# Kernel optimization log

Hardware: AMD Instinct MI355X
Metric: run time of the kernel (lower is better)

Reference implementation:

```python
import jax, jax.numpy as jnp
import numpy as np

B, H_IMG, W_IMG = 2, 192, 192
DIM, HEADS, WS, SHIFT = 192, 6, 8, 4
MLP_HID = 4 * DIM
EPS = 1e-5


def _rel_pos_index(ws):
    coords = np.stack(np.meshgrid(np.arange(ws), np.arange(ws), indexing='ij'))  # (2, ws, ws)
    cf = coords.reshape(2, -1)
    rel = (cf[:, :, None] - cf[:, None, :]).transpose(1, 2, 0)  # (ww, ww, 2)
    rel[:, :, 0] += ws - 1
    rel[:, :, 1] += ws - 1
    rel[:, :, 0] *= 2 * ws - 1
    return jnp.asarray(rel.sum(-1))  # (ww, ww) int


def _attn_mask(h, w, ws, shift):
    img = np.zeros((h, w))
    cnt = 0
    for hs in (slice(0, -ws), slice(-ws, -shift), slice(-shift, None)):
        for wsl in (slice(0, -ws), slice(-ws, -shift), slice(-shift, None)):
            img[hs, wsl] = cnt
            cnt += 1
    mw = img.reshape(h // ws, ws, w // ws, ws).transpose(0, 2, 1, 3).reshape(-1, ws * ws)
    am = mw[:, None, :] - mw[:, :, None]
    return jnp.asarray(np.where(am != 0, -100.0, 0.0), dtype=jnp.float32)


def setup_inputs() -> dict:
    key = jax.random.key(0)
    ks = jax.random.split(key, 16)
    n = H_IMG * W_IMG
    std = 0.02
    inp = {
        'x_left': jax.random.normal(ks[0], (B, n, DIM), jnp.float32),
        'x_right': jax.random.normal(ks[1], (B, n, DIM), jnp.float32),
        'd_left': jax.random.uniform(ks[2], (B, H_IMG, W_IMG), jnp.float32) * 8.0,
        'd_right': jax.random.uniform(ks[3], (B, H_IMG, W_IMG), jnp.float32) * 8.0,
        'norm1_g': jnp.ones((DIM,), jnp.float32),
        'norm1_b': jnp.zeros((DIM,), jnp.float32),
        'q_w': jax.random.normal(ks[4], (DIM, DIM), jnp.float32) * std,
        'q_b': jnp.zeros((DIM,), jnp.float32),
        'kv_w': jax.random.normal(ks[5], (DIM, 2 * DIM), jnp.float32) * std,
        'kv_b': jnp.zeros((2 * DIM,), jnp.float32),
        'proj_w': jax.random.normal(ks[6], (DIM, DIM), jnp.float32) * std,
        'proj_b': jnp.zeros((DIM,), jnp.float32),
        'rel_bias_table': jax.random.normal(ks[7], ((2 * WS - 1) ** 2, HEADS), jnp.float32) * std,
        'norm2_g': jnp.ones((DIM,), jnp.float32),
        'norm2_b': jnp.zeros((DIM,), jnp.float32),
        'fc1_w': jax.random.normal(ks[8], (DIM, MLP_HID), jnp.float32) * std,
        'fc1_b': jnp.zeros((MLP_HID,), jnp.float32),
        'fc2_w': jax.random.normal(ks[9], (MLP_HID, DIM), jnp.float32) * std,
        'fc2_b': jnp.zeros((DIM,), jnp.float32),
        'h': H_IMG,
        'w': W_IMG,
    }
    return inp


def _forward(x_left, x_right, d_left, d_right,
             norm1_g, norm1_b, q_w, q_b, kv_w, kv_b, proj_w, proj_b,
             rel_bias_table, norm2_g, norm2_b, fc1_w, fc1_b, fc2_w, fc2_b,
             h, w):
    b, n, c = x_left.shape
    ws, shift, heads = WS, SHIFT, HEADS
    hd = c // heads
    scale = hd ** -0.5
    ww = ws * ws
    nW = (h // ws) * (w // ws)

    rel_idx = _rel_pos_index(ws)
    # (heads, ww, ww) gathered relative-position bias
    bias = rel_bias_table[rel_idx.reshape(-1)].reshape(ww, ww, heads).transpose(2, 0, 1)
    mask = _attn_mask(h, w, ws, shift)  # (nW, ww, ww)

    coords_w = jnp.arange(w, dtype=jnp.float32)[None, None, :]
    r2l = jnp.clip(coords_w + 0.5 - d_left, 0.0, None).astype(jnp.int32)
    l2r = jnp.clip(coords_w + 0.5 + d_right, None, float(w - 1)).astype(jnp.int32)

    def ln(x, g, bt):
        mu = x.mean(-1, keepdims=True)
        var = ((x - mu) ** 2).mean(-1, keepdims=True)
        return (x - mu) / jnp.sqrt(var + EPS) * g + bt

    sc_l, sc_r = x_left, x_right
    xl = ln(x_left, norm1_g, norm1_b).reshape(b, h, w, c)
    xr = ln(x_right, norm1_g, norm1_b).reshape(b, h, w, c)
    # epipolar gather along width
    xl_sel = jnp.take_along_axis(xl, l2r[..., None], axis=2)
    xr_sel = jnp.take_along_axis(xr, r2l[..., None], axis=2)

    def shift_f(x):
        return jnp.roll(x, (-shift, -shift), axis=(1, 2))

    def part(x):  # window partition -> (b*nW, ww, c)
        x = x.reshape(b, h // ws, ws, w // ws, ws, c).transpose(0, 1, 3, 2, 4, 5)
        return x.reshape(-1, ww, c)

    xlw, xrw = part(shift_f(xl)), part(shift_f(xr))
    xlsw, xrsw = part(shift_f(xl_sel)), part(shift_f(xr_sel))

    def win_attn(xq, xkv):
        B_ = xq.shape[0]
        q = (xq @ q_w + q_b).reshape(B_, ww, heads, hd).transpose(0, 2, 1, 3) * scale
        kv = (xkv @ kv_w + kv_b).reshape(B_, ww, 2, heads, hd).transpose(2, 0, 3, 1, 4)
        k, v = kv[0], kv[1]
        a = jnp.einsum('bhqd,bhkd->bhqk', q, k) + bias[None]
        a = a.reshape(B_ // nW, nW, heads, ww, ww) + mask[None, :, None]
        a = jax.nn.softmax(a.reshape(B_, heads, ww, ww), axis=-1)
        o = jnp.einsum('bhqk,bhkd->bqhd', a, v).reshape(B_, ww, c)
        return o @ proj_w + proj_b, a

    xlT, a_r2l = win_attn(xlw, xrsw)
    xrT, a_l2r = win_attn(xrw, xlsw)

    def m_relax(M, p=2):  # sum over +-p shifts along the query axis
        out = M
        for i in range(1, p + 1):
            out = out + jnp.pad(M[:, :, :-i, :], ((0, 0), (0, 0), (i, 0), (0, 0)))
            out = out + jnp.pad(M[:, :, i:, :], ((0, 0), (0, 0), (0, i), (0, 0)))
        return out

    m_l = jnp.einsum('bhik,bhki->bhi', m_relax(a_r2l), a_l2r)
    m_r = jnp.einsum('bhik,bhki->bhi', m_relax(a_l2r), a_r2l)
    m_l = jax.lax.stop_gradient(jnp.tanh(5.0 * m_l.transpose(0, 2, 1)[..., None]))  # (B_, ww, heads, 1)
    m_r = jax.lax.stop_gradient(jnp.tanh(5.0 * m_r.transpose(0, 2, 1)[..., None]))

    def fuse(x_orig, x_t, m):
        B_ = x_orig.shape[0]
        xo = x_orig.reshape(B_, ww, heads, hd)
        xt = x_t.reshape(B_, ww, heads, hd)
        return (xo * (1.0 - m) + xt * m).reshape(B_, ww, c)

    xlT = fuse(xlw, xlT, m_l)
    xrT = fuse(xrw, xrT, m_r)

    def rev(win):  # window reverse + roll back
        x = win.reshape(b, h // ws, w // ws, ws, ws, c).transpose(0, 1, 3, 2, 4, 5).reshape(b, h, w, c)
        return jnp.roll(x, (shift, shift), axis=(1, 2))

    xl_out = sc_l + rev(xlT).reshape(b, n, c)
    xr_out = sc_r + rev(xrT).reshape(b, n, c)

    def mlp(x):
        return jax.nn.gelu(x @ fc1_w + fc1_b, approximate=False) @ fc2_w + fc2_b

    xl_out = xl_out + mlp(ln(xl_out, norm2_g, norm2_b))
    xr_out = xr_out + mlp(ln(xr_out, norm2_g, norm2_b))
    return xl_out, xr_out


def reference(x_left, x_right, d_left, d_right,
              norm1_g, norm1_b, q_w, q_b, kv_w, kv_b, proj_w, proj_b,
              rel_bias_table, norm2_g, norm2_b, fc1_w, fc1_b, fc2_w, fc2_b,
              h, w):
    return _forward(x_left, x_right, d_left, d_right,
                    norm1_g, norm1_b, q_w, q_b, kv_w, kv_b, proj_w, proj_b,
                    rel_bias_table, norm2_g, norm2_b, fc1_w, fc1_b, fc2_w, fc2_b,
                    h, w)
```

## Files before the change

### kernel.cpp

```cpp
#include <hip/hip_runtime.h>
#include <hip/hip_bf16.h>

#define BB 2
#define HH 192
#define WIMG 192
#define CC 192
#define NHEADS 6
#define HD 32
#define NTOK (HH*WIMG)
#define NWX 24
#define NWIN 576
#define BWIN (BB*NWIN)
#define MLPH 768
#define EPS_ 1e-5f
#define NSIDE_TOK (BB*NTOK)

typedef __attribute__((ext_vector_type(8))) short bf16x8;
typedef __attribute__((ext_vector_type(4))) float f32x4;

#define GLOBAL_AS __attribute__((address_space(1)))
#define LDS_AS __attribute__((address_space(3)))
__device__ __forceinline__ void gll16(const void* g, void* l) {
    __builtin_amdgcn_global_load_lds((const GLOBAL_AS unsigned int*)g,
                                     (LDS_AS unsigned int*)l, 16, 0, 0);
}

__device__ __forceinline__ unsigned short f2bf(float f) {
    __hip_bfloat16 h = __float2bfloat16(f);
    return *reinterpret_cast<unsigned short*>(&h);
}
__device__ __forceinline__ float bfu(unsigned short u) {
    return __uint_as_float(((unsigned int)u) << 16);
}
__device__ __forceinline__ float gelu_fast(float x) {
    float z = 1.5957691216f*(x + 0.044715f*x*x*x);
    float e = __expf(z);
    float t = 1.0f - 2.0f/(e + 1.0f);
    return 0.5f*x*(1.0f + t);
}
__device__ __forceinline__ int tokof(int b, int wi, int wj, int p) {
    int rh = wi*8 + (p>>3), rw = wj*8 + (p&7);
    int i = rh + 4; if (i >= HH) i -= HH;
    int j = rw + 4; if (j >= WIMG) j -= WIMG;
    return b*NTOK + i*WIMG + j;
}

__global__ __launch_bounds__(256) void ln1_kernel(
    const float* __restrict__ xl, const float* __restrict__ xr,
    const float* __restrict__ g, const float* __restrict__ bta,
    __hip_bfloat16* __restrict__ xln_all)
{
    int token = blockIdx.x*4 + (threadIdx.x >> 6);
    int lane = threadIdx.x & 63;
    const float* src;
    __hip_bfloat16* dst;
    if (token < NSIDE_TOK) { src = xl + (size_t)token*CC; dst = xln_all + (size_t)token*CC; }
    else { int t2 = token - NSIDE_TOK; src = xr + (size_t)t2*CC; dst = xln_all + (size_t)token*CC; }
    float v0 = src[lane], v1 = src[lane+64], v2 = src[lane+128];
    float s = v0+v1+v2;
    float q = v0*v0 + v1*v1 + v2*v2;
    #pragma unroll
    for (int m = 32; m; m >>= 1) { s += __shfl_xor(s, m, 64); q += __shfl_xor(q, m, 64); }
    float mu = s * (1.0f/CC);
    float inv = rsqrtf(fmaxf(q*(1.0f/CC) - mu*mu, 0.0f) + EPS_);
    dst[lane]     = __float2bfloat16((v0-mu)*inv*g[lane]     + bta[lane]);
    dst[lane+64]  = __float2bfloat16((v1-mu)*inv*g[lane+64]  + bta[lane+64]);
    dst[lane+128] = __float2bfloat16((v2-mu)*inv*g[lane+128] + bta[lane+128]);
}

__global__ __launch_bounds__(256) void map_kernel(
    const float* __restrict__ d_left, const float* __restrict__ d_right,
    int* __restrict__ map)
{
    int gid = blockIdx.x*256 + threadIdx.x;
    int side = (gid >= NSIDE_TOK) ? 1 : 0;
    int row = gid - side*NSIDE_TOK;
    int j = row % WIMG;
    float d = side ? d_right[row] : d_left[row];
    int jj;
    if (!side) { float f = (float)j + 0.5f - d; f = fmaxf(f, 0.f); jj = (int)f; }
    else       { float f = (float)j + 0.5f + d; f = fminf(f, 191.f); jj = (int)f; }
    map[gid] = (side ? 0 : NSIDE_TOK) + row - j + jj;
}

__global__ __launch_bounds__(256) void conv_w_kernel(
    const float* __restrict__ q_w, const float* __restrict__ kv_w,
    const float* __restrict__ proj_w, const float* __restrict__ fc1_w,
    const float* __restrict__ fc2_w,
    __hip_bfloat16* __restrict__ q_wf, __hip_bfloat16* __restrict__ kv_wf,
    __hip_bfloat16* __restrict__ proj_f, __hip_bfloat16* __restrict__ W1f,
    __hip_bfloat16* __restrict__ W2f)
{
    int idx = blockIdx.x*256 + threadIdx.x;
    if (idx < 36864) {
        int j = idx & 7, lane = (idx>>3) & 63, fr = idx>>9;
        int ct = fr % 12, ks = fr / 12;
        int n = ct*16 + (lane&15), k = ks*32 + (lane>>4)*8 + j;
        q_wf[idx] = __float2bfloat16(q_w[(size_t)k*192 + n]);
    } else if (idx < 110592) {
        int i2 = idx - 36864;
        int j = i2 & 7, lane = (i2>>3) & 63, fr = i2>>9;
        int ct = fr % 24, ks = fr / 24;
        int n = ct*16 + (lane&15), k = ks*32 + (lane>>4)*8 + j;
        kv_wf[i2] = __float2bfloat16(kv_w[(size_t)k*384 + n]);
    } else if (idx < 147456) {
        int i2 = idx - 110592;
        int j = i2 & 7, lane = (i2>>3) & 63, fr = i2>>9;
        int ct = fr % 12, h = fr / 12;
        int n = ct*16 + (lane&15), k = h*32 + (lane>>4)*8 + j;
        proj_f[i2] = __float2bfloat16(proj_w[(size_t)k*192 + n]);
    } else if (idx < 294912) {
        int i2 = idx - 147456;
        int j = i2 & 7, lane = (i2>>3) & 63, fr = i2>>9;
        int ct = fr & 1, ks = (fr>>1) % 6, cc2 = fr / 12;
        int n = cc2*32 + ct*16 + (lane&15), k = ks*32 + (lane>>4)*8 + j;
        W1f[i2] = __float2bfloat16(fc1_w[(size_t)k*MLPH + n]);
    } else {
        int i2 = idx - 294912;
        int j = i2 & 7, lane = (i2>>3) & 63, fr = i2>>9;
        int ct = fr % 12, ks = (fr/12) % 2, cc = fr / 24;
        int n = ct*16 + (lane&15), k = cc*64 + ks*32 + (lane>>4)*8 + j;
        W2f[i2] = __float2bfloat16(fc2_w[(size_t)k*192 + n]);
    }
}

__global__ __launch_bounds__(256) void bias_setup_kernel(
    const float* __restrict__ table, float* __restrict__ bias_glob)
{
    int idx = blockIdx.x*256 + threadIdx.x;
    int h = idx >> 12, rem = idx & 4095;
    int q = rem >> 6, k = rem & 63;
    int qy = q>>3, qx = q&7, ky = k>>3, kx = k&7;
    int ridx = (qy-ky+7)*15 + (qx-kx+7);
    bias_glob[idx] = table[ridx*NHEADS + h];
}

template<int NT>
__global__ __launch_bounds__(256) void proj_gemm_kernel(
    const __hip_bfloat16* __restrict__ in, const __hip_bfloat16* __restrict__ Wf,
    const float* __restrict__ bias, const int* __restrict__ map,
    __hip_bfloat16* __restrict__ outp, float scale)
{
    __shared__ unsigned short wst[2][NT*512];
    const int tid = threadIdx.x, lane = tid & 63, w = tid >> 6;
    const int r16 = lane & 15, kg = lane >> 4, w16 = w*16;
    const size_t baserow = (size_t)blockIdx.x * 64;
    const int row = (int)baserow + w16 + r16;
    const size_t arow = map ? (size_t)map[row] : (size_t)row;

    bf16x8 aReg[6];
    #pragma unroll
    for (int ks = 0; ks < 6; ++ks)
        aReg[ks] = *reinterpret_cast<const bf16x8*>(in + arow*CC + ks*32 + kg*8);

    const char* wsrc = (const char*)Wf;
    const int soff = w*1024 + lane*16;
    #pragma unroll
    for (int i = 0; i < NT/4; ++i)
        gll16(wsrc + i*4096 + soff, (char*)wst[0] + i*4096 + w*1024);

    f32x4 acc[NT];
    #pragma unroll
    for (int ct = 0; ct < NT; ++ct) { float bv = bias[ct*16+r16]; acc[ct] = (f32x4){bv,bv,bv,bv}; }

    #pragma unroll
    for (int ks = 0; ks < 6; ++ks) {
        __syncthreads();
        if (ks < 5) {
            const char* s2 = wsrc + (size_t)(ks+1)*NT*1024;
            #pragma unroll
            for (int i = 0; i < NT/4; ++i)
                gll16(s2 + i*4096 + soff, (char*)wst[(ks+1)&1] + i*4096 + w*1024);
        }
        #pragma unroll
        for (int ct = 0; ct < NT; ++ct) {
            bf16x8 bb = *reinterpret_cast<const bf16x8*>(wst[ks&1] + ct*512 + lane*8);
            acc[ct] = __builtin_amdgcn_mfma_f32_16x16x32_bf16(aReg[ks], bb, acc[ct], 0, 0, 0);
        }
    }
    const int ldo = NT*16;
    #pragma unroll
    for (int ct = 0; ct < NT; ++ct)
        #pragma unroll
        for (int r = 0; r < 4; ++r)
            outp[(baserow + w16 + kg*4 + r)*ldo + ct*16 + r16] =
                __float2bfloat16(acc[ct][r] * scale);
}

__global__ __launch_bounds__(128) void attn_pm_kernel(
    const __hip_bfloat16* __restrict__ Qglob,
    const __hip_bfloat16* __restrict__ KVglob,
    const float* __restrict__ bias_glob,
    __hip_bfloat16* __restrict__ Og,
    float* __restrict__ mg)
{
    __shared__ unsigned short Pl[2][64*72];
    __shared__ unsigned short Vl[2][32*72];
    const int tid = threadIdx.x, lane = tid & 63, s = tid >> 6;
    const int r16 = lane & 15, kg = lane >> 4;
    const int bid = blockIdx.x;
    const int wd = bid / NHEADS, h = bid % NHEADS;
    const int b = wd / NWIN, win = wd % NWIN;
    const int wi = win / NWX, wj = win % NWX;
    const bool edge_i = (wi == NWX-1), edge_j = (wj == NWX-1);

    const __hip_bfloat16* Qs  = Qglob  + (size_t)s*NSIDE_TOK*CC;
    const __hip_bfloat16* KVs = KVglob + (size_t)s*NSIDE_TOK*(2*CC);

    int tokQ[4];
    #pragma unroll
    for (int mi = 0; mi < 4; ++mi) tokQ[mi] = tokof(b, wi, wj, mi*16 + r16);
    const int tokV = tokof(b, wi, wj, lane);

    unsigned short* P = Pl[s];
    unsigned short* V = Vl[s];

    {
        bf16x8 vv[4];
        #pragma unroll
        for (int dg = 0; dg < 4; ++dg)
            vv[dg] = *reinterpret_cast<const bf16x8*>(
                KVs + (size_t)tokV*(2*CC) + CC + h*HD + dg*8);
        #pragma unroll
        for (int dg = 0; dg < 4; ++dg)
            #pragma unroll
            for (int jj = 0; jj < 8; ++jj)
                V[(dg*8+jj)*72 + lane] = (unsigned short)vv[dg][jj];
    }

    bf16x8 aQ[4], bK[4];
    #pragma unroll
    for (int mi = 0; mi < 4; ++mi)
        aQ[mi] = *reinterpret_cast<const bf16x8*>(
            Qs + (size_t)tokQ[mi]*CC + h*HD + kg*8);
    #pragma unroll
    for (int ni = 0; ni < 4; ++ni)
        bK[ni] = *reinterpret_cast<const bf16x8*>(
            KVs + (size_t)tokQ[ni]*(2*CC) + h*HD + kg*8);
    f32x4 S[4][4];
    #pragma unroll
    for (int mi = 0; mi < 4; ++mi)
        #pragma unroll
        for (int ni = 0; ni < 4; ++ni)
            S[mi][ni] = __builtin_amdgcn_mfma_f32_16x16x32_bf16(
                aQ[mi], bK[ni], (f32x4){0.f,0.f,0.f,0.f}, 0, 0, 0);

    #pragma unroll
    for (int mi = 0; mi < 4; ++mi)
        #pragma unroll
        for (int ni = 0; ni < 4; ++ni)
            #pragma unroll
            for (int rr = 0; rr < 4; ++rr) {
                int q = mi*16 + kg*4 + rr, k = ni*16 + r16;
                float bm = bias_glob[h*4096 + q*64 + k];
                int qy = q>>3, qx = q&7, ky = k>>3, kx = k&7;
                bool msk = (edge_i && ((qy<4) != (ky<4))) ||
                           (edge_j && ((qx<4) != (kx<4)));
                S[mi][ni][rr] += bm + (msk ? -100.0f : 0.0f);
            }

    float mx[4][4], sm[4][4];
    #pragma unroll
    for (int mi = 0; mi < 4; ++mi)
        #pragma unroll
        for (int rr = 0; rr < 4; ++rr)
            mx[mi][rr] = fmaxf(fmaxf(S[mi][0][rr], S[mi][1][rr]),
                               fmaxf(S[mi][2][rr], S[mi][3][rr]));
    #pragma unroll
    for (int m = 1; m <= 8; m <<= 1)
        #pragma unroll
        for (int mi = 0; mi < 4; ++mi)
            #pragma unroll
            for (int rr = 0; rr < 4; ++rr)
                mx[mi][rr] = fmaxf(mx[mi][rr], __shfl_xor(mx[mi][rr], m, 64));
    #pragma unroll
    for (int mi = 0; mi < 4; ++mi)
        #pragma unroll
        for (int rr = 0; rr < 4; ++rr) sm[mi][rr] = 0.f;
    #pragma unroll
    for (int mi = 0; mi < 4; ++mi)
        #pragma unroll
        for (int ni = 0; ni < 4; ++ni)
            #pragma unroll
            for (int rr = 0; rr < 4; ++rr) {
                S[mi][ni][rr] = __expf(S[mi][ni][rr] - mx[mi][rr]);
                sm[mi][rr] += S[mi][ni][rr];
            }
    #pragma unroll
    for (int m = 1; m <= 8; m <<= 1)
        #pragma unroll
        for (int mi = 0; mi < 4; ++mi)
            #pragma unroll
            for (int rr = 0; rr < 4; ++rr)
                sm[mi][rr] += __shfl_xor(sm[mi][rr], m, 64);
    #pragma unroll
    for (int mi = 0; mi < 4; ++mi)
        #pragma unroll
        for (int rr = 0; rr < 4; ++rr) sm[mi][rr] = 1.0f / sm[mi][rr];

    #pragma unroll
    for (int mi = 0; mi < 4; ++mi)
        #pragma unroll
        for (int ni = 0; ni < 4; ++ni)
            #pragma unroll
            for (int rr = 0; rr < 4; ++rr)
                P[(mi*16 + kg*4 + rr)*72 + ni*16 + r16] =
                    f2bf(S[mi][ni][rr] * sm[mi][rr]);

    {
        f32x4 O[4][2];
        #pragma unroll
        for (int mi = 0; mi < 4; ++mi)
            #pragma unroll
            for (int dt = 0; dt < 2; ++dt) O[mi][dt] = (f32x4){0.f,0.f,0.f,0.f};
        #pragma unroll
        for (int ks = 0; ks < 2; ++ks) {
            bf16x8 aP[4], bV[2];
            #pragma unroll
            for (int mi = 0; mi < 4; ++mi)
                aP[mi] = *reinterpret_cast<const bf16x8*>(
                    P + (mi*16 + r16)*72 + ks*32 + kg*8);
            #pragma unroll
            for (int dt = 0; dt < 2; ++dt)
                bV[dt] = *reinterpret_cast<const bf16x8*>(
                    V + (dt*16 + r16)*72 + ks*32 + kg*8);
            #pragma unroll
            for (int mi = 0; mi < 4; ++mi)
                #pragma unroll
                for (int dt = 0; dt < 2; ++dt)
                    O[mi][dt] = __builtin_amdgcn_mfma_f32_16x16x32_bf16(
                        aP[mi], bV[dt], O[mi][dt], 0, 0, 0);
        }
        __hip_bfloat16* ob = Og + ((size_t)(s*BWIN + wd)*64)*CC + h*HD;
        #pragma unroll
        for (int mi = 0; mi < 4; ++mi)
            #pragma unroll
            for (int dt = 0; dt < 2; ++dt)
                #pragma unroll
                for (int rr = 0; rr < 4; ++rr)
                    ob[(size_t)(mi*16 + kg*4 + rr)*CC + dt*16 + r16] =
                        __float2bfloat16(O[mi][dt][rr]);
    }

    __syncthreads();

    {
        const unsigned short* Pa = Pl[s];
        const unsigned short* Pb = Pl[s^1];
        const int i = lane;
        const int s0 = (i >= 2) ? -2 : -i;
        const int s1 = (i <= 61) ? 2 : 63 - i;
        float acc = 0.f;
        for (int k = 0; k < 64; k += 2) {
            float pb0 = bfu(Pb[k*72 + i]);
            float pb1 = bfu(Pb[(k+1)*72 + i]);
            float a0 = 0.f, a1 = 0.f;
            for (int ss = s0; ss <= s1; ++ss) {
                unsigned int pr = *reinterpret_cast<const unsigned int*>(
                    &Pa[(i+ss)*72 + k]);
                a0 += bfu((unsigned short)(pr & 0xffff));
                a1 += bfu((unsigned short)(pr >> 16));
            }
            acc += a0*pb0 + a1*pb1;
        }
        float e = __expf(10.0f * acc);
        mg[((size_t)(s*BWIN + wd)*NHEADS + h)*64 + i] = 1.0f - 2.0f/(e + 1.0f);
    }
}

__global__ __launch_bounds__(256) void projfuse_kernel(
    const __hip_bfloat16* __restrict__ Og,
    const __hip_bfloat16* __restrict__ proj_f,
    const float* __restrict__ proj_b,
    const float* __restrict__ mg,
    const __hip_bfloat16* __restrict__ xln_all,
    const float* __restrict__ x_left, const float* __restrict__ x_right,
    const float* __restrict__ g2, const float* __restrict__ b2,
    float* __restrict__ out, __hip_bfloat16* __restrict__ xln2)
{
    __shared__ unsigned short wst[2][12*512];
    const int tid = threadIdx.x, lane = tid & 63, w = tid >> 6;
    const int r16 = lane & 15, kg = lane >> 4, w16 = w*16;
    const int bid = blockIdx.x;
    const int s = bid / BWIN, wd = bid % BWIN;
    const int b = wd / NWIN, win = wd % NWIN;
    const int wi = win / NWX, wj = win % NWX;

    const size_t orow = (size_t)(s*BWIN + wd)*64 + w16 + r16;
    bf16x8 aReg[6];
    #pragma unroll
    for (int ks = 0; ks < 6; ++ks)
        aReg[ks] = *reinterpret_cast<const bf16x8*>(Og + orow*CC + ks*32 + kg*8);

    const char* wsrc = (const char*)proj_f;
    const int soff = w*1024 + lane*16;
    #pragma unroll
    for (int i = 0; i < 3; ++i)
        gll16(wsrc + i*4096 + soff, (char*)wst[0] + i*4096 + w*1024);

    f32x4 acc[12];
    #pragma unroll
    for (int ct = 0; ct < 12; ++ct) { float bv = proj_b[ct*16+r16]; acc[ct] = (f32x4){bv,bv,bv,bv}; }

    #pragma unroll
    for (int ks = 0; ks < 6; ++ks) {
        __syncthreads();
        if (ks < 5) {
            const char* s2 = wsrc + (size_t)(ks+1)*12288;
            #pragma unroll
            for (int i = 0; i < 3; ++i)
                gll16(s2 + i*4096 + soff, (char*)wst[(ks+1)&1] + i*4096 + w*1024);
        }
        #pragma unroll
        for (int ct = 0; ct < 12; ++ct) {
            bf16x8 bb = *reinterpret_cast<const bf16x8*>(wst[ks&1] + ct*512 + lane*8);
            acc[ct] = __builtin_amdgcn_mfma_f32_16x16x32_bf16(aReg[ks], bb, acc[ct], 0, 0, 0);
        }
    }

    int tk[4];
    #pragma unroll
    for (int rr = 0; rr < 4; ++rr) tk[rr] = tokof(b, wi, wj, w16 + kg*4 + rr);
    const float* xo_s = s ? x_right : x_left;
    const __hip_bfloat16* xw_s = xln_all + (size_t)s*NSIDE_TOK*CC;
    float* out_s = out + (size_t)s*NSIDE_TOK*CC;
    __hip_bfloat16* xln2_s = xln2 + (size_t)s*NSIDE_TOK*CC;
    const float* mrow = mg + (size_t)(s*BWIN + wd)*NHEADS*64;

    float g2c[12], b2c[12];
    #pragma unroll
    for (int ct = 0; ct < 12; ++ct) {
        g2c[ct] = g2[ct*16 + r16];
        b2c[ct] = b2[ct*16 + r16];
    }

    #pragma unroll
    for (int ct = 0; ct < 12; ++ct) {
        int col = ct*16 + r16;
        int h = ct >> 1;
        #pragma unroll
        for (int rr = 0; rr < 4; ++rr) {
            int q = w16 + kg*4 + rr;
            size_t tt = (size_t)tk[rr];
            float m = mrow[h*64 + q];
            float xw = __bfloat162float(xw_s[tt*CC + col]);
            float p = acc[ct][rr];
            float val = xo_s[tt*CC + col] + xw + (p - xw)*m;
            out_s[tt*CC + col] = val;
            acc[ct][rr] = val;
        }
    }

    #pragma unroll
    for (int rr = 0; rr < 4; ++rr) {
        float sum = 0.f, sq = 0.f;
        #pragma unroll
        for (int ct = 0; ct < 12; ++ct) {
            float v = acc[ct][rr];
            sum += v; sq += v*v;
        }
        #pragma unroll
        for (int m = 1; m <= 8; m <<= 1) {
            sum += __shfl_xor(sum, m, 64);
            sq  += __shfl_xor(sq,  m, 64);
        }
        float mu = sum * (1.0f/CC);
        float inv = rsqrtf(fmaxf(sq*(1.0f/CC) - mu*mu, 0.0f) + EPS_);
        size_t tt = (size_t)tk[rr];
        #pragma unroll
        for (int ct = 0; ct < 12; ++ct) {
            unsigned short uv = f2bf((acc[ct][rr]-mu)*inv*g2c[ct] + b2c[ct]);
            *reinterpret_cast<unsigned short*>(&xln2_s[tt*CC + ct*16 + r16]) = uv;
        }
    }
}

__global__ __launch_bounds__(256) void mlp_mfma_kernel(
    float* __restrict__ out, const __hip_bfloat16* __restrict__ xln2,
    const __hip_bfloat16* __restrict__ W1f, const float* __restrict__ fc1_b,
    const __hip_bfloat16* __restrict__ W2f, const float* __restrict__ fc2_b)
{
    __shared__ unsigned short hbuf[64*72];
    __shared__ unsigned short wst[2][6144];
    const int tid  = threadIdx.x;
    const int lane = tid & 63;
    const int w    = tid >> 6;
    const int r16 = lane & 15, kg = lane >> 4, w16 = w*16;
    const size_t base = (size_t)blockIdx.x * 64 * CC;

    bf16x8 aReg[6];
    #pragma unroll
    for (int ks = 0; ks < 6; ++ks)
        aReg[ks] = *reinterpret_cast<const bf16x8*>(
            xln2 + base + (size_t)(w16 + r16)*CC + ks*32 + kg*8);

    const char* W1c = (const char*)W1f;
    const char* W2c = (const char*)W2f;
    const int soff = w*1024 + lane*16;
    const int doff = w*1024;

    #pragma unroll
    for (int i = 0; i < 3; ++i)
        gll16(W1c + i*4096 + soff, (char*)wst[0] + i*4096 + doff);

    f32x4 acc2[12];
    #pragma unroll
    for (int i = 0; i < 12; ++i) acc2[i] = (f32x4){0.f,0.f,0.f,0.f};

    for (int cc = 0; cc < 12; ++cc) {
        f32x4 acc1[4];
        __builtin_amdgcn_s_barrier();
        {
            const char* s2 = W1c + (size_t)(2*cc+1)*12288;
            #pragma unroll
            for (int i = 0; i < 3; ++i)
                gll16(s2 + i*4096 + soff, (char*)wst[1] + i*4096 + doff);
        }
        asm volatile("s_waitcnt vmcnt(3)" ::: "memory");
        __builtin_amdgcn_s_barrier();
        #pragma unroll
        for (int c2 = 0; c2 < 2; ++c2) {
            float bv = fc1_b[cc*64 + c2*16 + r16];
            acc1[c2] = (f32x4){bv,bv,bv,bv};
        }
        #pragma unroll
        for (int ks = 0; ks < 6; ++ks)
            #pragma unroll
            for (int c2 = 0; c2 < 2; ++c2) {
                bf16x8 bw = *reinterpret_cast<const bf16x8*>(wst[0] + (ks*2+c2)*512 + lane*8);
                acc1[c2] = __builtin_amdgcn_mfma_f32_16x16x32_bf16(aReg[ks], bw, acc1[c2], 0, 0, 0);
            }
        __builtin_amdgcn_s_barrier();
        {
            const char* s2 = W2c + (size_t)(2*cc)*12288;
            #pragma unroll
            for (int i = 0; i < 3; ++i)
                gll16(s2 + i*4096 + soff, (char*)wst[0] + i*4096 + doff);
        }
        asm volatile("s_waitcnt vmcnt(3)" ::: "memory");
        __builtin_amdgcn_s_barrier();
        #pragma unroll
        for (int c2 = 0; c2 < 2; ++c2) {
            float bv = fc1_b[cc*64 + 32 + c2*16 + r16];
            acc1[2+c2] = (f32x4){bv,bv,bv,bv};
        }
        #pragma unroll
        for (int ks = 0; ks < 6; ++ks)
            #pragma unroll
            for (int c2 = 0; c2 < 2; ++c2) {
                bf16x8 bw = *reinterpret_cast<const bf16x8*>(wst[1] + (ks*2+c2)*512 + lane*8);
                acc1[2+c2] = __builtin_amdgcn_mfma_f32_16x16x32_bf16(aReg[ks], bw, acc1[2+c2], 0, 0, 0);
            }
        #pragma unroll
        for (int ct = 0; ct < 4; ++ct)
            #pragma unroll
            for (int r = 0; r < 4; ++r)
                hbuf[(w16 + kg*4 + r)*72 + ct*16 + r16] = f2bf(gelu_fast(acc1[ct][r]));
        __builtin_amdgcn_s_barrier();
        {
            const char* s2 = W2c + (size_t)(2*cc+1)*12288;
            #pragma unroll
            for (int i = 0; i < 3; ++i)
                gll16(s2 + i*4096 + soff, (char*)wst[1] + i*4096 + doff);
        }
        asm volatile("s_waitcnt vmcnt(3)" ::: "memory");
        __builtin_amdgcn_s_barrier();
        {
            bf16x8 aP = *reinterpret_cast<const bf16x8*>(hbuf + (w16+r16)*72 + kg*8);
            #pragma unroll
            for (int ct = 0; ct < 12; ++ct) {
                bf16x8 bw = *reinterpret_cast<const bf16x8*>(wst[0] + ct*512 + lane*8);
                acc2[ct] = __builtin_amdgcn_mfma_f32_16x16x32_bf16(aP, bw, acc2[ct], 0, 0, 0);
            }
        }
        __builtin_amdgcn_s_barrier();
        if (cc < 11) {
            const char* s2 = W1c + (size_t)(2*cc+2)*12288;
            #pragma unroll
            for (int i = 0; i < 3; ++i)
                gll16(s2 + i*4096 + soff, (char*)wst[0] + i*4096 + doff);
            asm volatile("s_waitcnt vmcnt(3)" ::: "memory");
        } else {
            asm volatile("s_waitcnt vmcnt(0)" ::: "memory");
        }
        __builtin_amdgcn_s_barrier();
        {
            bf16x8 aP = *reinterpret_cast<const bf16x8*>(hbuf + (w16+r16)*72 + 32 + kg*8);
            #pragma unroll
            for (int ct = 0; ct < 12; ++ct) {
                bf16x8 bw = *reinterpret_cast<const bf16x8*>(wst[1] + ct*512 + lane*8);
                acc2[ct] = __builtin_amdgcn_mfma_f32_16x16x32_bf16(aP, bw, acc2[ct], 0, 0, 0);
            }
        }
    }

    #pragma unroll
    for (int ct = 0; ct < 12; ++ct) {
        int col = ct*16 + r16;
        float bv = fc2_b[col];
        #pragma unroll
        for (int r = 0; r < 4; ++r) {
            size_t idx = base + (size_t)(w16 + kg*4 + r)*CC + col;
            out[idx] = out[idx] + acc2[ct][r] + bv;
        }
    }
}

extern "C" void kernel_launch(void* const* d_in, const int* in_sizes, int n_in,
                              void* d_out, int out_size, void* d_ws, size_t ws_size,
                              hipStream_t stream)
{
    (void)in_sizes; (void)n_in; (void)out_size; (void)ws_size;
    const float* x_left  = (const float*)d_in[0];
    const float* x_right = (const float*)d_in[1];
    const float* d_left  = (const float*)d_in[2];
    const float* d_right = (const float*)d_in[3];
    const float* n1g = (const float*)d_in[4];
    const float* n1b = (const float*)d_in[5];
    const float* q_w = (const float*)d_in[6];
    const float* q_b = (const float*)d_in[7];
    const float* kv_w = (const float*)d_in[8];
    const float* kv_b = (const float*)d_in[9];
    const float* proj_w = (const float*)d_in[10];
    const float* proj_b = (const float*)d_in[11];
    const float* bias_table = (const float*)d_in[12];
    const float* n2g = (const float*)d_in[13];
    const float* n2b = (const float*)d_in[14];
    const float* fc1_w = (const float*)d_in[15];
    const float* fc1_b = (const float*)d_in[16];
    const float* fc2_w = (const float*)d_in[17];
    const float* fc2_b = (const float*)d_in[18];
    float* out = (float*)d_out;

    char* ws = (char*)d_ws;
    __hip_bfloat16* xln_all  = (__hip_bfloat16*)(ws);
    __hip_bfloat16* Qg       = (__hip_bfloat16*)(ws + 56623104);
    __hip_bfloat16* KVg      = (__hip_bfloat16*)(ws + 113246208);
    __hip_bfloat16* xln2     = (__hip_bfloat16*)(ws + 113246208);
    __hip_bfloat16* q_wf     = (__hip_bfloat16*)(ws + 226492416);
    __hip_bfloat16* kv_wf    = (__hip_bfloat16*)(ws + 226566144);
    __hip_bfloat16* proj_f   = (__hip_bfloat16*)(ws + 226713600);
    __hip_bfloat16* W1f      = (__hip_bfloat16*)(ws + 226787328);
    __hip_bfloat16* W2f      = (__hip_bfloat16*)(ws + 227082240);
    float*          bias_g   = (float*)         (ws + 227377152);
    __hip_bfloat16* Og       = (__hip_bfloat16*)(ws + 227770368);
    int*            map      = (int*)           (ws + 284393472);
    float*          mg       = (float*)         (ws + 284983296);

    ln1_kernel<<<(2*NSIDE_TOK)/4, 256, 0, stream>>>(x_left, x_right, n1g, n1b, xln_all);

    conv_w_kernel<<<1728, 256, 0, stream>>>(q_w, kv_w, proj_w, fc1_w, fc2_w,
                                            q_wf, kv_wf, proj_f, W1f, W2f);
    bias_setup_kernel<<<96, 256, 0, stream>>>(bias_table, bias_g);
    map_kernel<<<(2*NSIDE_TOK)/256, 256, 0, stream>>>(d_left, d_right, map);

    proj_gemm_kernel<24><<<(2*NSIDE_TOK)/64, 256, 0, stream>>>(
        xln_all, kv_wf, kv_b, map, KVg, 1.0f);
    proj_gemm_kernel<12><<<(2*NSIDE_TOK)/64, 256, 0, stream>>>(
        xln_all, q_wf, q_b, nullptr, Qg, 0.17677669529663687f);

    attn_pm_kernel<<<BWIN*NHEADS, 128, 0, stream>>>(Qg, KVg, bias_g, Og, mg);

    projfuse_kernel<<<2*BWIN, 256, 0, stream>>>(
        Og, proj_f, proj_b, mg, xln_all, x_left, x_right, n2g, n2b, out, xln2);

    mlp_mfma_kernel<<<(2*NSIDE_TOK)/64, 256, 0, stream>>>(
        out, xln2, W1f, fc1_b, W2f, fc2_b);
}
```

Baseline: 536.8 us.

## Switch MLP kernel to 32x32x16 MFMA tiles with 2x2 wave split

Rewrites the fused MLP kernel to use 32x32x16 bf16 MFMA instead of 16x16x32. The four waves now form a 2x2 grid over rows and output columns rather than each wave owning 16 rows. Weight fragments are repacked to match, and staging chunks double so each hidden-chunk iteration loads fc1 and fc2 slabs once, halving barrier rounds. This aims to raise MFMA efficiency and reduce LDS reads per FLOP, at the cost of doubled LDS staging buffers, which may lower occupancy.

New measurement: 549.5 us. 1.02x slower.

```diff
diff --git a/kernel.cpp b/kernel.cpp
--- a/kernel.cpp
+++ b/kernel.cpp
@@ -17,6 +17,7 @@
 
 typedef __attribute__((ext_vector_type(8))) short bf16x8;
 typedef __attribute__((ext_vector_type(4))) float f32x4;
+typedef __attribute__((ext_vector_type(16))) float f32x16;
 
 #define GLOBAL_AS __attribute__((address_space(1)))
 #define LDS_AS __attribute__((address_space(3)))
@@ -111,15 +112,17 @@
         proj_f[i2] = __float2bfloat16(proj_w[(size_t)k*192 + n]);
     } else if (idx < 294912) {
         int i2 = idx - 147456;
-        int j = i2 & 7, lane = (i2>>3) & 63, fr = i2>>9;
-        int ct = fr & 1, ks = (fr>>1) % 6, cc2 = fr / 12;
-        int n = cc2*32 + ct*16 + (lane&15), k = ks*32 + (lane>>4)*8 + j;
+        int j = i2 & 7, l = (i2>>3) & 63, fr = i2>>9;
+        int cc = fr / 24, r = fr % 24;
+        int ch = r / 12, ks = r % 12;
+        int n = cc*64 + ch*32 + (l&31), k = ks*16 + (l>>5)*8 + j;
         W1f[i2] = __float2bfloat16(fc1_w[(size_t)k*MLPH + n]);
     } else {
         int i2 = idx - 294912;
-        int j = i2 & 7, lane = (i2>>3) & 63, fr = i2>>9;
-        int ct = fr % 12, ks = (fr/12) % 2, cc = fr / 24;
-        int n = ct*16 + (lane&15), k = cc*64 + ks*32 + (lane>>4)*8 + j;
+        int j = i2 & 7, l = (i2>>3) & 63, fr = i2>>9;
+        int cc = fr / 24, r = fr % 24;
+        int ct6 = r / 4, ks = r % 4;
+        int n = ct6*32 + (l&31), k = cc*64 + ks*16 + (l>>5)*8 + j;
         W2f[i2] = __float2bfloat16(fc2_w[(size_t)k*192 + n]);
     }
 }
@@ -481,18 +484,20 @@
     const __hip_bfloat16* __restrict__ W2f, const float* __restrict__ fc2_b)
 {
     __shared__ unsigned short hbuf[64*72];
-    __shared__ unsigned short wst[2][6144];
+    __shared__ unsigned short wst[2][12288];
     const int tid  = threadIdx.x;
     const int lane = tid & 63;
     const int w    = tid >> 6;
-    const int r16 = lane & 15, kg = lane >> 4, w16 = w*16;
+    const int c32 = lane & 31, kg2 = lane >> 5;
+    const int rt = w & 1, ch = w >> 1;
     const size_t base = (size_t)blockIdx.x * 64 * CC;
-
-    bf16x8 aReg[6];
-    #pragma unroll
-    for (int ks = 0; ks < 6; ++ks)
+    const int arow = rt*32 + c32;
+
+    bf16x8 aReg[12];
+    #pragma unroll
+    for (int ks = 0; ks < 12; ++ks)
         aReg[ks] = *reinterpret_cast<const bf16x8*>(
-            xln2 + base + (size_t)(w16 + r16)*CC + ks*32 + kg*8);
+            xln2 + base + (size_t)arow*CC + ks*16 + kg2*8);
 
     const char* W1c = (const char*)W1f;
     const char* W2c = (const char*)W2f;
@@ -500,108 +505,79 @@
     const int doff = w*1024;
 
     #pragma unroll
-    for (int i = 0; i < 3; ++i)
+    for (int i = 0; i < 6; ++i)
         gll16(W1c + i*4096 + soff, (char*)wst[0] + i*4096 + doff);
 
-    f32x4 acc2[12];
-    #pragma unroll
-    for (int i = 0; i < 12; ++i) acc2[i] = (f32x4){0.f,0.f,0.f,0.f};
+    f32x16 acc2[3];
+    #pragma unroll
+    for (int t3 = 0; t3 < 3; ++t3)
+        #pragma unroll
+        for (int r = 0; r < 16; ++r) acc2[t3][r] = 0.f;
 
     for (int cc = 0; cc < 12; ++cc) {
-        f32x4 acc1[4];
         __builtin_amdgcn_s_barrier();
         {
-            const char* s2 = W1c + (size_t)(2*cc+1)*12288;
-            #pragma unroll
-            for (int i = 0; i < 3; ++i)
+            const char* s2 = W2c + (size_t)cc*24576;
+            #pragma unroll
+            for (int i = 0; i < 6; ++i)
                 gll16(s2 + i*4096 + soff, (char*)wst[1] + i*4096 + doff);
         }
-        asm volatile("s_waitcnt vmcnt(3)" ::: "memory");
+        asm volatile("s_waitcnt vmcnt(6)" ::: "memory");
         __builtin_amdgcn_s_barrier();
-        #pragma unroll
-        for (int c2 = 0; c2 < 2; ++c2) {
-            float bv = fc1_b[cc*64 + c2*16 + r16];
-            acc1[c2] = (f32x4){bv,bv,bv,bv};
-        }
-        #pragma unroll
-        for (int ks = 0; ks < 6; ++ks)
-            #pragma unroll
-            for (int c2 = 0; c2 < 2; ++c2) {
-                bf16x8 bw = *reinterpret_cast<const bf16x8*>(wst[0] + (ks*2+c2)*512 + lane*8);
-                acc1[c2] = __builtin_amdgcn_mfma_f32_16x16x32_bf16(aReg[ks], bw, acc1[c2], 0, 0, 0);
-            }
-        __builtin_amdgcn_s_barrier();
+        f32x16 acc1;
         {
-            const char* s2 = W2c + (size_t)(2*cc)*12288;
-            #pragma unroll
-            for (int i = 0; i < 3; ++i)
-                gll16(s2 + i*4096 + soff, (char*)wst[0] + i*4096 + doff);
-        }
-        asm volatile("s_waitcnt vmcnt(3)" ::: "memory");
-        __builtin_amdgcn_s_barrier();
-        #pragma unroll
-        for (int c2 = 0; c2 < 2; ++c2) {
-            float bv = fc1_b[cc*64 + 32 + c2*16 + r16];
-            acc1[2+c2] = (f32x4){bv,bv,bv,bv};
-        }
-        #pragma unroll
-        for (int ks = 0; ks < 6; ++ks)
-            #pragma unroll
-            for (int c2 = 0; c2 < 2; ++c2) {
-                bf16x8 bw = *reinterpret_cast<const bf16x8*>(wst[1] + (ks*2+c2)*512 + lane*8);
-                acc1[2+c2] = __builtin_amdgcn_mfma_f32_16x16x32_bf16(aReg[ks], bw, acc1[2+c2], 0, 0, 0);
-            }
-        #pragma unroll
-        for (int ct = 0; ct < 4; ++ct)
-            #pragma unroll
-            for (int r = 0; r < 4; ++r)
-                hbuf[(w16 + kg*4 + r)*72 + ct*16 + r16] = f2bf(gelu_fast(acc1[ct][r]));
-        __builtin_amdgcn_s_barrier();
-        {
-            const char* s2 = W2c + (size_t)(2*cc+1)*12288;
-            #pragma unroll
-            for (int i = 0; i < 3; ++i)
-                gll16(s2 + i*4096 + soff, (char*)wst[1] + i*4096 + doff);
-        }
-        asm volatile("s_waitcnt vmcnt(3)" ::: "memory");
-        __builtin_amdgcn_s_barrier();
-        {
-            bf16x8 aP = *reinterpret_cast<const bf16x8*>(hbuf + (w16+r16)*72 + kg*8);
-            #pragma unroll
-            for (int ct = 0; ct < 12; ++ct) {
-                bf16x8 bw = *reinterpret_cast<const bf16x8*>(wst[0] + ct*512 + lane*8);
-                acc2[ct] = __builtin_amdgcn_mfma_f32_16x16x32_bf16(aP, bw, acc2[ct], 0, 0, 0);
-            }
+            float bv = fc1_b[cc*64 + ch*32 + c32];
+            #pragma unroll
+            for (int r = 0; r < 16; ++r) acc1[r] = bv;
+        }
+        #pragma unroll
+        for (int ks = 0; ks < 12; ++ks) {
+            bf16x8 bw = *reinterpret_cast<const bf16x8*>(
+                wst[0] + (ch*12 + ks)*512 + lane*8);
+            acc1 = __builtin_amdgcn_mfma_f32_32x32x16_bf16(aReg[ks], bw, acc1, 0, 0, 0);
+        }
+        #pragma unroll
+        for (int r = 0; r < 16; ++r) {
+            int row = rt*32 + (r&3) + 8*(r>>2) + 4*kg2;
+            hbuf[row*72 + ch*32 + c32] = f2bf(gelu_fast(acc1[r]));
         }
         __builtin_amdgcn_s_barrier();
         if (cc < 11) {
-            const char* s2 = W1c + (size_t)(2*cc+2)*12288;
-            #pragma unroll
-            for (int i = 0; i < 3; ++i)
+            const char* s2 = W1c + (size_t)(cc+1)*24576;
+            #pragma unroll
+            for (int i = 0; i < 6; ++i)
                 gll16(s2 + i*4096 + soff, (char*)wst[0] + i*4096 + doff);
-            asm volatile("s_waitcnt vmcnt(3)" ::: "memory");
+            asm volatile("s_waitcnt vmcnt(6)" ::: "memory");
         } else {
             asm volatile("s_waitcnt vmcnt(0)" ::: "memory");
         }
         __builtin_amdgcn_s_barrier();
-        {
-            bf16x8 aP = *reinterpret_cast<const bf16x8*>(hbuf + (w16+r16)*72 + 32 + kg*8);
-            #pragma unroll
-            for (int ct = 0; ct < 12; ++ct) {
-                bf16x8 bw = *reinterpret_cast<const bf16x8*>(wst[1] + ct*512 + lane*8);
-                acc2[ct] = __builtin_amdgcn_mfma_f32_16x16x32_bf16(aP, bw, acc2[ct], 0, 0, 0);
+        bf16x8 aH[4];
+        #pragma unroll
+        for (int ks = 0; ks < 4; ++ks)
+            aH[ks] = *reinterpret_cast<const bf16x8*>(
+                hbuf + arow*72 + ks*16 + kg2*8);
+        #pragma unroll
+        for (int t3 = 0; t3 < 3; ++t3) {
+            const int ct6 = ch*3 + t3;
+            #pragma unroll
+            for (int ks = 0; ks < 4; ++ks) {
+                bf16x8 bw = *reinterpret_cast<const bf16x8*>(
+                    wst[1] + (ct6*4 + ks)*512 + lane*8);
+                acc2[t3] = __builtin_amdgcn_mfma_f32_32x32x16_bf16(aH[ks], bw, acc2[t3], 0, 0, 0);
             }
         }
     }
 
     #pragma unroll
-    for (int ct = 0; ct < 12; ++ct) {
-        int col = ct*16 + r16;
-        float bv = fc2_b[col];
-        #pragma unroll
-        for (int r = 0; r < 4; ++r) {
-            size_t idx = base + (size_t)(w16 + kg*4 + r)*CC + col;
-            out[idx] = out[idx] + acc2[ct][r] + bv;
+    for (int t3 = 0; t3 < 3; ++t3) {
+        int colb = (ch*3 + t3)*32 + c32;
+        float bv = fc2_b[colb];
+        #pragma unroll
+        for (int r = 0; r < 16; ++r) {
+            int row = rt*32 + (r&3) + 8*(r>>2) + 4*kg2;
+            size_t idx = base + (size_t)row*CC + colb;
+            out[idx] = out[idx] + acc2[t3][r] + bv;
         }
     }
 }
```
